# Optimization experiments

Hardware: AMD Instinct MI355X
Metric: run time of the kernel (lower is better)

## Reference

```python
import jax, jax.numpy as jnp
import numpy as np

B, T = 128, 512
V, E, H, A, L = 50000, 256, 512, 64, 2


def setup_inputs() -> dict:
    key = jax.random.key(0)
    ks = jax.random.split(key, 16)
    token_ids = jax.random.randint(ks[0], (B, T), 0, V, dtype=jnp.int32)
    # lengths must be >= 2 so that the source's (len-1)-1 index is valid
    lengths = jnp.clip(jax.random.randint(ks[1], (B,), 0, T, dtype=jnp.int32), 4, T)
    s = 0.05
    inp = {
        "token_ids": token_ids,
        "lengths": lengths,
        "embedding": jax.random.normal(ks[2], (V, E), jnp.float32) * s,
        "Wt": jax.random.normal(ks[3], (A, E), jnp.float32) * s,   # tokens_linear
        "bt": jax.random.normal(ks[4], (A,), jnp.float32) * s,
        "Wq": jax.random.normal(ks[5], (A, H), jnp.float32) * s,   # query_linear
        "bq": jax.random.normal(ks[6], (A,), jnp.float32) * s,
        "v": jax.random.normal(ks[7], (A,), jnp.float32) * s,      # attention_linear weight
        "bv": jax.random.normal(ks[8], (), jnp.float32) * s,       # attention_linear bias
        "gru_Wih0": jax.random.normal(ks[9], (3 * H, A), jnp.float32) * s,
        "gru_Whh0": jax.random.normal(ks[10], (3 * H, H), jnp.float32) * s,
        "gru_bih0": jax.random.normal(ks[11], (3 * H,), jnp.float32) * s,
        "gru_bhh0": jax.random.normal(ks[12], (3 * H,), jnp.float32) * s,
        "gru_Wih1": jax.random.normal(ks[13], (3 * H, H), jnp.float32) * s,
        "gru_Whh1": jax.random.normal(ks[14], (3 * H, H), jnp.float32) * s,
        "gru_bih1": jax.random.normal(ks[15], (3 * H,), jnp.float32) * s,
        "gru_bhh1": jax.random.normal(jax.random.fold_in(key, 99), (3 * H,), jnp.float32) * s,
    }
    return inp


def _gru_cell(x, h, Wih, Whh, bih, bhh):
    gi = x @ Wih.T + bih      # [B, 3H]
    gh = h @ Whh.T + bhh      # [B, 3H]
    i_r, i_z, i_n = jnp.split(gi, 3, axis=-1)
    h_r, h_z, h_n = jnp.split(gh, 3, axis=-1)
    r = jax.nn.sigmoid(i_r + h_r)
    z = jax.nn.sigmoid(i_z + h_z)
    n = jnp.tanh(i_n + r * h_n)
    return (1.0 - z) * n + z * h


def reference(token_ids, lengths, embedding, Wt, bt, Wq, bq, v, bv,
              gru_Wih0, gru_Whh0, gru_bih0, gru_bhh0,
              gru_Wih1, gru_Whh1, gru_bih1, gru_bhh1):
    x = embedding[token_ids]                 # [B, T, E]
    tp = jnp.einsum('bte,ae->bta', x, Wt) + bt   # tokens_linear, [B, T, A]
    pos = jnp.arange(T)

    def step(h, i):
        # query = hidden_state[-1] (zeros at step 0, matching hidden_state=None)
        q = h[-1] @ Wq.T + bq                # [B, A]
        s = jnp.tanh(tp + q[:, None, :]) @ v + bv   # [B, T]
        s = jnp.where(pos[None, :] <= i, s, -jnp.inf)  # growing prefix
        attn = jax.nn.softmax(s, axis=1)
        ctx = jnp.einsum('bt,bta->ba', attn, tp)     # [B, A]
        h0 = _gru_cell(ctx, h[0], gru_Wih0, gru_Whh0, gru_bih0, gru_bhh0)
        h1 = _gru_cell(h0, h[1], gru_Wih1, gru_Whh1, gru_bih1, gru_bhh1)
        return jnp.stack([h0, h1]), h1

    h_init = jnp.zeros((L, B, H), tp.dtype)
    _, outs = jax.lax.scan(step, h_init, jnp.arange(T))   # outs: [T, B, H]
    # source: sequence_lengths = len-1, then index sequence_lengths-1 = len-2
    idx = jnp.clip(lengths - 2, 0, T - 1)
    result = outs[idx, jnp.arange(B)]                     # [B, H]
    return result
```

## Files before the change

kernel.cpp:

```cpp
#include <hip/hip_runtime.h>

#define NB 128
#define NT 512
#define NE 256
#define NH 512
#define NA 64
#define NG 8
#define GB 16

typedef short bf16x8 __attribute__((ext_vector_type(8)));
typedef float f32x4 __attribute__((ext_vector_type(4)));
typedef unsigned short u16x8 __attribute__((ext_vector_type(8)));
typedef unsigned long long u64;

__device__ __forceinline__ unsigned short f2bf(float f){
  unsigned u = __builtin_bit_cast(unsigned, f);
  u = u + 0x7fffu + ((u >> 16) & 1u);
  return (unsigned short)(u >> 16);
}
__device__ __forceinline__ float bf2f(unsigned short h){
  unsigned u = ((unsigned)h) << 16;
  return __builtin_bit_cast(float, u);
}
__device__ __forceinline__ bf16x8 packbf2(f32x4 a, f32x4 b){
  bf16x8 r;
  r[0]=(short)f2bf(a[0]); r[1]=(short)f2bf(a[1]); r[2]=(short)f2bf(a[2]); r[3]=(short)f2bf(a[3]);
  r[4]=(short)f2bf(b[0]); r[5]=(short)f2bf(b[1]); r[6]=(short)f2bf(b[2]); r[7]=(short)f2bf(b[3]);
  return r;
}
__device__ __forceinline__ bf16x8 loadB_f32(const float* p){
  f32x4 a = *(const f32x4*)p;
  f32x4 b = *(const f32x4*)(p + 4);
  return packbf2(a, b);
}
#define MFMA(a,b,c) __builtin_amdgcn_mfma_f32_16x16x32_bf16(a,b,c,0,0,0)

__device__ __forceinline__ float fsig(float x){
  return __builtin_amdgcn_rcpf(1.f + __expf(-x));
}
__device__ __forceinline__ float ftanh(float x){
  float e2 = __expf(2.f * x);
  return 1.f - 2.f * __builtin_amdgcn_rcpf(e2 + 1.f);
}

__device__ __forceinline__ void sleep_bk(int bk){
  if (bk <= 0)      __builtin_amdgcn_s_sleep(1);
  else if (bk == 1) __builtin_amdgcn_s_sleep(2);
  else if (bk == 2) __builtin_amdgcn_s_sleep(4);
  else              __builtin_amdgcn_s_sleep(8);
}

__device__ __forceinline__ u64 aload(const u64* p){
  return __hip_atomic_load(p, __ATOMIC_RELAXED, __HIP_MEMORY_SCOPE_AGENT);
}
__device__ __forceinline__ void fire(u64* p, u64 v){
  (void)__hip_atomic_exchange(p, v, __ATOMIC_RELAXED, __HIP_MEMORY_SCOPE_AGENT);
}
__device__ __forceinline__ u64 packh(unsigned sq, float a, float b){
  return ((u64)sq << 32) | ((u64)f2bf(b) << 16) | (u64)f2bf(a);
}
__device__ __forceinline__ u64 packf(unsigned sq, float a){
  return ((u64)sq << 32) | (u64)__builtin_bit_cast(unsigned, a);
}

__global__ __launch_bounds__(256) void k_tp(
    const int* __restrict__ tok, const float* __restrict__ emb,
    const float* __restrict__ Wt, const float* __restrict__ bt,
    unsigned short* __restrict__ tp)
{
  const int lane = threadIdx.x & 63;
  const int w = threadIdx.x >> 6;
  const int m16 = lane & 15, quad = lane >> 4;

  bf16x8 wfq[8][4];
#pragma unroll
  for (int kc = 0; kc < 8; kc++)
#pragma unroll
    for (int nt = 0; nt < 4; nt++)
      wfq[kc][nt] = loadB_f32(Wt + (nt*16 + m16)*NE + kc*32 + quad*8);

  float btv[4];
#pragma unroll
  for (int nt = 0; nt < 4; nt++) btv[nt] = bt[nt*16 + m16];

  const int gw = blockIdx.x * 4 + w;
#pragma unroll 1
  for (int it = 0; it < 4; it++){
    const int pt = gw * 4 + it;
    const int pos = pt*16 + m16;
    const long row = (long)tok[pos];
    const float* xrow = emb + row * NE;
    f32x4 acc[4] = {{0,0,0,0},{0,0,0,0},{0,0,0,0},{0,0,0,0}};
#pragma unroll
    for (int kc = 0; kc < 8; kc++){
      bf16x8 af = loadB_f32(xrow + kc*32 + quad*8);
#pragma unroll
      for (int nt = 0; nt < 4; nt++)
        acc[nt] = MFMA(af, wfq[kc][nt], acc[nt]);
    }
#pragma unroll
    for (int nt = 0; nt < 4; nt++)
#pragma unroll
      for (int r = 0; r < 4; r++){
        int posr = pt*16 + quad*4 + r;
        tp[(long)posr * NA + nt*16 + m16] = f2bf(acc[nt][r] + btv[nt]);
      }
  }
}

__global__ __launch_bounds__(256) void k_pack(
    const float* __restrict__ Wq, unsigned short* __restrict__ blob)
{
  const int lane = threadIdx.x & 63, wv = threadIdx.x >> 6;
  const int m16 = lane & 15, quad = lane >> 4;
#pragma unroll
  for (int kc = 0; kc < 16; kc++){
    bf16x8 t = loadB_f32(Wq + (long)(wv*16 + m16)*NH + kc*32 + quad*8);
    *(bf16x8*)&blob[((wv*16 + kc)*64 + lane)*8] = t;
  }
}

struct KArgs {
  const int* len;
  const float* bq; const float* v; const float* bv;
  const float* Wih0; const float* Whh0; const float* bih0; const float* bhh0;
  const float* Wih1; const float* Whh1; const float* bih1; const float* bhh1;
  const unsigned short* tp;
  const unsigned short* wqblob;
  u64* hbuf;
  u64* cbuf;
  float* out;
};

__device__ __forceinline__ void stage_load(const u64* __restrict__ buf, unsigned sq,
                                           unsigned short (*hs)[64][8], int tid){
  const int lane = tid & 63, wv = tid >> 6;
  const int b = lane & 15, q8 = lane >> 4;
#pragma unroll
  for (int c = 0; c < 4; c++){
    const int kc = wv*4 + c;
    const u64* u0 = buf + (kc*4 + q8)*64 + b*4;
    u64 x0, x1, x2, x3;
    int bk = 0;
    for (;;){
      x0 = aload(u0);     x1 = aload(u0 + 1);
      x2 = aload(u0 + 2); x3 = aload(u0 + 3);
      if ((unsigned)(x0>>32)==sq && (unsigned)(x1>>32)==sq &&
          (unsigned)(x2>>32)==sq && (unsigned)(x3>>32)==sq) break;
      sleep_bk(bk);
      if (bk < 3) bk++;
    }
    u16x8 d;
    d[0]=(unsigned short)x0; d[1]=(unsigned short)(x0>>16);
    d[2]=(unsigned short)x1; d[3]=(unsigned short)(x1>>16);
    d[4]=(unsigned short)x2; d[5]=(unsigned short)(x2>>16);
    d[6]=(unsigned short)x3; d[7]=(unsigned short)(x3>>16);
    *(u16x8*)&hs[kc][lane][0] = d;
  }
}

__global__ __launch_bounds__(256, 1) void k_main(KArgs A_)
{
  const int tid = threadIdx.x, lane = tid & 63, w = tid >> 6;
  const int g = blockIdx.x & 7, m = blockIdx.x >> 3;
  const int m16 = lane & 15, quad = lane >> 4;

  __shared__ __attribute__((aligned(16))) unsigned short h0s[16][64][8];
  __shared__ __attribute__((aligned(16))) unsigned short h1s[16][64][8];
  __shared__ __attribute__((aligned(16))) float dslab[6][256];
  __shared__ __attribute__((aligned(16))) float qs[16][68];
  __shared__ __attribute__((aligned(16))) float cslab[4][64];
  __shared__ float cden[4];
  __shared__ __attribute__((aligned(16))) unsigned short ctxf[64][16];

  u64* hb = A_.hbuf + (long)g * (4*4096);
  u64* cb = A_.cbuf + (long)g * (2*2*16*72);
  const int b0 = g * GB;

  bf16x8 wf[48], wih0f[2];
  float bhh0v[4], bih0v[4], bhh1v[4], bih1v[4];
  if (w < 3){
    const int r0 = w * NH + m * 16;
#pragma unroll
    for (int kc = 0; kc < 16; kc++){
      wf[kc]    = loadB_f32(A_.Whh0 + (long)(r0 + m16)*NH + kc*32 + quad*8);
      wf[16+kc] = loadB_f32(A_.Whh1 + (long)(r0 + m16)*NH + kc*32 + quad*8);
      wf[32+kc] = loadB_f32(A_.Wih1 + (long)(r0 + m16)*NH + kc*32 + quad*8);
    }
#pragma unroll
    for (int kc = 0; kc < 2; kc++)
      wih0f[kc] = loadB_f32(A_.Wih0 + (r0 + m16)*NA + kc*32 + quad*8);
#pragma unroll
    for (int r = 0; r < 4; r++){
      int d = r0 + quad*4 + r;
      bhh0v[r] = A_.bhh0[d]; bih0v[r] = A_.bih0[d];
      bhh1v[r] = A_.bhh1[d]; bih1v[r] = A_.bih1[d];
    }
  }
  float bqw[4];
#pragma unroll
  for (int r = 0; r < 4; r++) bqw[r] = A_.bq[w*16 + quad*4 + r];

  float vv[16];
#pragma unroll
  for (int jj = 0; jj < 16; jj++) vv[jj] = A_.v[quad*16 + jj];
  const float bvv = A_.bv[0];
  const int ab = m >> 1;
  const int wr = (m & 1)*4 + w;

  int myidx = 0, imax = 0;
#pragma unroll 1
  for (int b = 0; b < GB; b++){
    int L = A_.len[b0 + b];
    int ix = L - 2; ix = ix < 0 ? 0 : (ix > NT-1 ? NT-1 : ix);
    if (b == m16) myidx = ix;
    imax = imax > ix ? imax : ix;
  }

  f32x4 h0p = {0,0,0,0}, h1p = {0,0,0,0};

  {
    u16x8 z = {0,0,0,0,0,0,0,0};
#pragma unroll
    for (int c = 0; c < 4; c++){
      int kc = (tid>>6)*4 + c;
      *(u16x8*)&h0s[kc][lane][0] = z;
      *(u16x8*)&h1s[kc][lane][0] = z;
    }
  }
  __syncthreads();

#pragma unroll 1
  for (int i = 0; i <= imax; i++){
    const int par = i & 1;
    const unsigned sq = (unsigned)(i + 1);

    f32x4 g0 = {0,0,0,0};
    if (w < 3){
#pragma unroll
      for (int kc = 0; kc < 16; kc++){
        bf16x8 h0f = *(const bf16x8*)&h0s[kc][lane][0];
        g0 = MFMA(wf[kc], h0f, g0);
      }
#pragma unroll
      for (int r = 0; r < 4; r++) g0[r] += bhh0v[r];
    }
    if (i > 0){
      stage_load(hb + (long)(2 + ((i-1)&1))*4096, (unsigned)i, h1s, tid);
      __syncthreads();
    }
    {
      f32x4 qa = {0,0,0,0};
#pragma unroll
      for (int kc = 0; kc < 16; kc++){
        bf16x8 b1f = *(const bf16x8*)&h1s[kc][lane][0];
        bf16x8 af = *(const bf16x8*)&A_.wqblob[((w*16 + kc)*64 + lane)*8];
        qa = MFMA(af, b1f, qa);
      }
#pragma unroll
      for (int r = 0; r < 4; r++)
        qs[m16][w*16 + quad*4 + r] = qa[r] + bqw[r];
    }
    __syncthreads();

    {
      float qv[16];
#pragma unroll
      for (int jq = 0; jq < 4; jq++){
        f32x4 t = *(const f32x4*)&qs[ab][quad*16 + jq*4];
        qv[jq*4+0]=t[0]; qv[jq*4+1]=t[1]; qv[jq*4+2]=t[2]; qv[jq*4+3]=t[3];
      }
      float ctxp[16];
#pragma unroll
      for (int jj = 0; jj < 16; jj++) ctxp[jj] = 0.f;
      float denp = 0.f;
      const unsigned short* tpb = A_.tp + (long)(b0 + ab) * NT * NA;
#pragma unroll 1
      for (int c = wr; c*16 <= i; c += 8){
        const int t = c*16 + m16;
        const unsigned short* tpp = tpb + (long)t*NA + quad*16;
        u16x8 ta = *(const u16x8*)tpp;
        u16x8 tb = *(const u16x8*)(tpp + 8);
        float tpf[16];
#pragma unroll
        for (int jj = 0; jj < 8; jj++){ tpf[jj] = bf2f(ta[jj]); tpf[8+jj] = bf2f(tb[jj]); }
        float sp = 0.f;
#pragma unroll
        for (int jj = 0; jj < 16; jj++){
          float x = tpf[jj] + qv[jj];
          sp = fmaf(ftanh(x), vv[jj], sp);
        }
        sp += __shfl_xor(sp, 16);
        sp += __shfl_xor(sp, 32);
        float e = __expf(sp + bvv);
        e = (t <= i) ? e : 0.f;
        denp += e;
#pragma unroll
        for (int jj = 0; jj < 16; jj++) ctxp[jj] = fmaf(e, tpf[jj], ctxp[jj]);
      }
#pragma unroll
      for (int off = 1; off < 64; off <<= 1) denp += __shfl_xor(denp, off);
      denp *= 0.25f;
#pragma unroll
      for (int st = 0; st < 4; st++){
        const int bit = 1 << st;
        const bool up = (lane >> st) & 1;
        const int n2 = (16 >> st) >> 1;
#pragma unroll
        for (int j2 = 0; j2 < 8; j2++){
          if (j2 < n2){
            float keep = up ? ctxp[2*j2+1] : ctxp[2*j2];
            float send = up ? ctxp[2*j2]   : ctxp[2*j2+1];
            float got = __shfl_xor(send, bit);
            ctxp[j2] = keep + got;
          }
        }
      }
      cslab[w][lane] = ctxp[0];
      if (lane == 0) cden[w] = denp;
    }
    __syncthreads();
    if (w == 0){
      float s = cslab[0][lane] + cslab[1][lane] + cslab[2][lane] + cslab[3][lane];
      u64* slot = cb + ((long)(par*2 + (m & 1))*16 + ab)*72;
      fire(slot + lane, packf(sq, s));
      if (lane == 0)
        fire(slot + 64, packf(sq, cden[0]+cden[1]+cden[2]+cden[3]));
    }

    if (w == 3){
      const u64* c0 = cb + ((long)(par*2 + 0)*16 + m16)*72;
      const u64* c1 = cb + ((long)(par*2 + 1)*16 + m16)*72;
      u64 d0, d1;
      {
        int bk = 0;
        for (;;){
          d0 = aload(c0 + 64); d1 = aload(c1 + 64);
          if ((unsigned)(d0>>32)==sq && (unsigned)(d1>>32)==sq) break;
          sleep_bk(bk);
          if (bk < 3) bk++;
        }
      }
      const float rdn = __builtin_amdgcn_rcpf(
          __builtin_bit_cast(float,(unsigned)d0) + __builtin_bit_cast(float,(unsigned)d1));
#pragma unroll
      for (int kc = 0; kc < 2; kc++){
        const int a0 = kc*32 + quad*8;
        u64 t0[8], t1[8];
        int bk = 0;
        for (;;){
          bool ok = true;
#pragma unroll
          for (int j = 0; j < 8; j++){ t0[j] = aload(c0 + a0 + j); ok &= ((unsigned)(t0[j]>>32)==sq); }
#pragma unroll
          for (int j = 0; j < 8; j++){ t1[j] = aload(c1 + a0 + j); ok &= ((unsigned)(t1[j]>>32)==sq); }
          if (ok) break;
          sleep_bk(bk);
          if (bk < 3) bk++;
        }
        u16x8 f;
#pragma unroll
        for (int j = 0; j < 8; j++){
          float s = (__builtin_bit_cast(float,(unsigned)t0[j]) +
                     __builtin_bit_cast(float,(unsigned)t1[j])) * rdn;
          f[j] = f2bf(s);
        }
        *(u16x8*)&ctxf[lane][kc*8] = f;
      }
    }
    __syncthreads();
    if (w < 3){
      f32x4 gi0 = {0,0,0,0};
      bf16x8 cf0 = *(const bf16x8*)&ctxf[lane][0];
      bf16x8 cf1 = *(const bf16x8*)&ctxf[lane][8];
      gi0 = MFMA(wih0f[0], cf0, gi0);
      gi0 = MFMA(wih0f[1], cf1, gi0);
#pragma unroll
      for (int r = 0; r < 4; r++) gi0[r] += bih0v[r];
      *(f32x4*)&dslab[w][lane*4] = g0;
      *(f32x4*)&dslab[3+w][lane*4] = gi0;
    }
    __syncthreads();
    if (w == 3){
      f32x4 ghr = *(f32x4*)&dslab[0][lane*4];
      f32x4 ghz = *(f32x4*)&dslab[1][lane*4];
      f32x4 ghn = *(f32x4*)&dslab[2][lane*4];
      f32x4 gir = *(f32x4*)&dslab[3][lane*4];
      f32x4 giz = *(f32x4*)&dslab[4][lane*4];
      f32x4 gin = *(f32x4*)&dslab[5][lane*4];
      f32x4 hn;
#pragma unroll
      for (int r = 0; r < 4; r++){
        float rr = fsig(gir[r] + ghr[r]);
        float zz = fsig(giz[r] + ghz[r]);
        float nn = ftanh(gin[r] + rr*ghn[r]);
        hn[r] = (1.f - zz)*nn + zz*h0p[r];
      }
      h0p = hn;
      const int dp0 = m*8 + quad*2;
      u64* p0 = hb + (long)par*4096 + (dp0>>2)*64 + m16*4 + (dp0&3);
      fire(p0,     packh(sq, hn[0], hn[1]));
      fire(p0 + 1, packh(sq, hn[2], hn[3]));
    }

    f32x4 gh1 = {0,0,0,0};
    if (w < 3){
#pragma unroll
      for (int kc = 0; kc < 16; kc++){
        bf16x8 b1f = *(const bf16x8*)&h1s[kc][lane][0];
        gh1 = MFMA(wf[16+kc], b1f, gh1);
      }
#pragma unroll
      for (int r = 0; r < 4; r++) gh1[r] += bhh1v[r];
    }
    stage_load(hb + (long)par*4096, sq, h0s, tid);
    __syncthreads();
    if (w < 3){
      f32x4 gi1 = {0,0,0,0};
#pragma unroll
      for (int kc = 0; kc < 16; kc++){
        bf16x8 hf = *(const bf16x8*)&h0s[kc][lane][0];
        gi1 = MFMA(wf[32+kc], hf, gi1);
      }
#pragma unroll
      for (int r = 0; r < 4; r++) gi1[r] += bih1v[r];
      *(f32x4*)&dslab[w][lane*4] = gh1;
      *(f32x4*)&dslab[3+w][lane*4] = gi1;
    }
    __syncthreads();
    if (w == 3){
      f32x4 ghr = *(f32x4*)&dslab[0][lane*4];
      f32x4 ghz = *(f32x4*)&dslab[1][lane*4];
      f32x4 ghn = *(f32x4*)&dslab[2][lane*4];
      f32x4 gir = *(f32x4*)&dslab[3][lane*4];
      f32x4 giz = *(f32x4*)&dslab[4][lane*4];
      f32x4 gin = *(f32x4*)&dslab[5][lane*4];
      f32x4 hn;
#pragma unroll
      for (int r = 0; r < 4; r++){
        float rr = fsig(gir[r] + ghr[r]);
        float zz = fsig(giz[r] + ghz[r]);
        float nn = ftanh(gin[r] + rr*ghn[r]);
        hn[r] = (1.f - zz)*nn + zz*h1p[r];
      }
      h1p = hn;
      const int dp0 = m*8 + quad*2;
      u64* p1 = hb + (long)(2 + par)*4096 + (dp0>>2)*64 + m16*4 + (dp0&3);
      fire(p1,     packh(sq, hn[0], hn[1]));
      fire(p1 + 1, packh(sq, hn[2], hn[3]));
      if (i == myidx)
        *(f32x4*)&A_.out[(long)(b0 + m16)*NH + m*16 + quad*4] = hn;
    }
  }
}

extern "C" void kernel_launch(void* const* d_in, const int* in_sizes, int n_in,
                              void* d_out, int out_size, void* d_ws, size_t ws_size,
                              hipStream_t stream)
{
  (void)in_sizes; (void)n_in; (void)out_size; (void)ws_size;
  char* ws = (char*)d_ws;
  unsigned short* tp     = (unsigned short*)ws;
  unsigned short* wqblob = (unsigned short*)(ws + 8388608);
  u64* hbuf = (u64*)(ws + 8388608 + 65536);
  u64* cbuf = hbuf + 8 * (4*4096);

  (void)hipMemsetAsync(hbuf, 0xFF, (size_t)(8*4*4096 + 8*2*2*16*72) * sizeof(u64), stream);

  k_tp<<<dim3(256), dim3(256), 0, stream>>>(
      (const int*)d_in[0], (const float*)d_in[2], (const float*)d_in[3],
      (const float*)d_in[4], tp);
  k_pack<<<dim3(1), dim3(256), 0, stream>>>((const float*)d_in[5], wqblob);

  KArgs ka;
  ka.len  = (const int*)d_in[1];
  ka.bq   = (const float*)d_in[6];
  ka.v    = (const float*)d_in[7];  ka.bv   = (const float*)d_in[8];
  ka.Wih0 = (const float*)d_in[9];  ka.Whh0 = (const float*)d_in[10];
  ka.bih0 = (const float*)d_in[11]; ka.bhh0 = (const float*)d_in[12];
  ka.Wih1 = (const float*)d_in[13]; ka.Whh1 = (const float*)d_in[14];
  ka.bih1 = (const float*)d_in[15]; ka.bhh1 = (const float*)d_in[16];
  ka.tp = tp; ka.wqblob = wqblob;
  ka.hbuf = hbuf; ka.cbuf = cbuf;
  ka.out = (float*)d_out;

  k_main<<<dim3(256), dim3(256), 0, stream>>>(ka);
}
```

Measured before the change: 6.863 ms.

## Halve block count, double waves per block to cut cross-block context exchange

```diff
diff --git a/kernel.cpp b/kernel.cpp
--- a/kernel.cpp
+++ b/kernel.cpp
@@ -134,32 +134,37 @@
 
 __device__ __forceinline__ void stage_load(const u64* __restrict__ buf, unsigned sq,
                                            unsigned short (*hs)[64][8], int tid){
-  const int lane = tid & 63, wv = tid >> 6;
+  const int lane = tid & 63, w8 = tid >> 6;
   const int b = lane & 15, q8 = lane >> 4;
-#pragma unroll
-  for (int c = 0; c < 4; c++){
-    const int kc = wv*4 + c;
-    const u64* u0 = buf + (kc*4 + q8)*64 + b*4;
-    u64 x0, x1, x2, x3;
-    int bk = 0;
-    for (;;){
-      x0 = aload(u0);     x1 = aload(u0 + 1);
-      x2 = aload(u0 + 2); x3 = aload(u0 + 3);
-      if ((unsigned)(x0>>32)==sq && (unsigned)(x1>>32)==sq &&
-          (unsigned)(x2>>32)==sq && (unsigned)(x3>>32)==sq) break;
-      sleep_bk(bk);
-      if (bk < 3) bk++;
-    }
-    u16x8 d;
-    d[0]=(unsigned short)x0; d[1]=(unsigned short)(x0>>16);
-    d[2]=(unsigned short)x1; d[3]=(unsigned short)(x1>>16);
-    d[4]=(unsigned short)x2; d[5]=(unsigned short)(x2>>16);
-    d[6]=(unsigned short)x3; d[7]=(unsigned short)(x3>>16);
-    *(u16x8*)&hs[kc][lane][0] = d;
-  }
-}
-
-__global__ __launch_bounds__(256, 1) void k_main(KArgs A_)
+  const u64* uA = buf + ((w8*2+0)*4 + q8)*64 + b*4;
+  const u64* uB = buf + ((w8*2+1)*4 + q8)*64 + b*4;
+  u64 x[8];
+  int bk = 0;
+  for (;;){
+    bool ok = true;
+#pragma unroll
+    for (int j = 0; j < 4; j++) x[j]   = aload(uA + j);
+#pragma unroll
+    for (int j = 0; j < 4; j++) x[4+j] = aload(uB + j);
+#pragma unroll
+    for (int j = 0; j < 8; j++) ok &= ((unsigned)(x[j]>>32) == sq);
+    if (ok) break;
+    sleep_bk(bk);
+    if (bk < 3) bk++;
+  }
+  u16x8 dA, dB;
+#pragma unroll
+  for (int j = 0; j < 4; j++){
+    dA[2*j]   = (unsigned short)x[j];
+    dA[2*j+1] = (unsigned short)(x[j] >> 16);
+    dB[2*j]   = (unsigned short)x[4+j];
+    dB[2*j+1] = (unsigned short)(x[4+j] >> 16);
+  }
+  *(u16x8*)&hs[w8*2+0][lane][0] = dA;
+  *(u16x8*)&hs[w8*2+1][lane][0] = dB;
+}
+
+__global__ __launch_bounds__(512, 1) void k_main(KArgs A_)
 {
   const int tid = threadIdx.x, lane = tid & 63, w = tid >> 6;
   const int g = blockIdx.x & 7, m = blockIdx.x >> 3;
@@ -167,20 +172,20 @@
 
   __shared__ __attribute__((aligned(16))) unsigned short h0s[16][64][8];
   __shared__ __attribute__((aligned(16))) unsigned short h1s[16][64][8];
-  __shared__ __attribute__((aligned(16))) float dslab[6][256];
+  __shared__ __attribute__((aligned(16))) float dslab[6][512];
   __shared__ __attribute__((aligned(16))) float qs[16][68];
-  __shared__ __attribute__((aligned(16))) float cslab[4][64];
-  __shared__ float cden[4];
+  __shared__ __attribute__((aligned(16))) float cslab[8][64];
+  __shared__ float cden[8];
   __shared__ __attribute__((aligned(16))) unsigned short ctxf[64][16];
 
   u64* hb = A_.hbuf + (long)g * (4*4096);
-  u64* cb = A_.cbuf + (long)g * (2*2*16*72);
+  u64* cb = A_.cbuf + (long)g * (2*16*72);
   const int b0 = g * GB;
 
   bf16x8 wf[48], wih0f[2];
   float bhh0v[4], bih0v[4], bhh1v[4], bih1v[4];
-  if (w < 3){
-    const int r0 = w * NH + m * 16;
+  if (w < 6){
+    const int r0 = (w % 3) * NH + m * 32 + (w / 3) * 16;
 #pragma unroll
     for (int kc = 0; kc < 16; kc++){
       wf[kc]    = loadB_f32(A_.Whh0 + (long)(r0 + m16)*NH + kc*32 + quad*8);
@@ -199,14 +204,12 @@
   }
   float bqw[4];
 #pragma unroll
-  for (int r = 0; r < 4; r++) bqw[r] = A_.bq[w*16 + quad*4 + r];
+  for (int r = 0; r < 4; r++) bqw[r] = A_.bq[(w & 3)*16 + quad*4 + r];
 
   float vv[16];
 #pragma unroll
   for (int jj = 0; jj < 16; jj++) vv[jj] = A_.v[quad*16 + jj];
   const float bvv = A_.bv[0];
-  const int ab = m >> 1;
-  const int wr = (m & 1)*4 + w;
 
   int myidx = 0, imax = 0;
 #pragma unroll 1
@@ -222,8 +225,8 @@
   {
     u16x8 z = {0,0,0,0,0,0,0,0};
 #pragma unroll
-    for (int c = 0; c < 4; c++){
-      int kc = (tid>>6)*4 + c;
+    for (int c = 0; c < 2; c++){
+      int kc = w*2 + c;
       *(u16x8*)&h0s[kc][lane][0] = z;
       *(u16x8*)&h1s[kc][lane][0] = z;
     }
@@ -236,7 +239,7 @@
     const unsigned sq = (unsigned)(i + 1);
 
     f32x4 g0 = {0,0,0,0};
-    if (w < 3){
+    if (w < 6){
 #pragma unroll
       for (int kc = 0; kc < 16; kc++){
         bf16x8 h0f = *(const bf16x8*)&h0s[kc][lane][0];
@@ -245,11 +248,10 @@
 #pragma unroll
       for (int r = 0; r < 4; r++) g0[r] += bhh0v[r];
     }
-    if (i > 0){
+    if (i > 0)
       stage_load(hb + (long)(2 + ((i-1)&1))*4096, (unsigned)i, h1s, tid);
-      __syncthreads();
-    }
-    {
+    __syncthreads();
+    if (w < 4){
       f32x4 qa = {0,0,0,0};
 #pragma unroll
       for (int kc = 0; kc < 16; kc++){
@@ -267,16 +269,16 @@
       float qv[16];
 #pragma unroll
       for (int jq = 0; jq < 4; jq++){
-        f32x4 t = *(const f32x4*)&qs[ab][quad*16 + jq*4];
+        f32x4 t = *(const f32x4*)&qs[m][quad*16 + jq*4];
         qv[jq*4+0]=t[0]; qv[jq*4+1]=t[1]; qv[jq*4+2]=t[2]; qv[jq*4+3]=t[3];
       }
       float ctxp[16];
 #pragma unroll
       for (int jj = 0; jj < 16; jj++) ctxp[jj] = 0.f;
       float denp = 0.f;
-      const unsigned short* tpb = A_.tp + (long)(b0 + ab) * NT * NA;
+      const unsigned short* tpb = A_.tp + (long)(b0 + m) * NT * NA;
 #pragma unroll 1
-      for (int c = wr; c*16 <= i; c += 8){
+      for (int c = w; c*16 <= i; c += 8){
         const int t = c*16 + m16;
         const unsigned short* tpp = tpb + (long)t*NA + quad*16;
         u16x8 ta = *(const u16x8*)tpp;
@@ -321,55 +323,42 @@
     }
     __syncthreads();
     if (w == 0){
-      float s = cslab[0][lane] + cslab[1][lane] + cslab[2][lane] + cslab[3][lane];
-      u64* slot = cb + ((long)(par*2 + (m & 1))*16 + ab)*72;
+      float s = cslab[0][lane] + cslab[1][lane] + cslab[2][lane] + cslab[3][lane]
+              + cslab[4][lane] + cslab[5][lane] + cslab[6][lane] + cslab[7][lane];
+      u64* slot = cb + ((long)par*16 + m)*72;
       fire(slot + lane, packf(sq, s));
-      if (lane == 0)
-        fire(slot + 64, packf(sq, cden[0]+cden[1]+cden[2]+cden[3]));
-    }
-
-    if (w == 3){
-      const u64* c0 = cb + ((long)(par*2 + 0)*16 + m16)*72;
-      const u64* c1 = cb + ((long)(par*2 + 1)*16 + m16)*72;
-      u64 d0, d1;
-      {
-        int bk = 0;
-        for (;;){
-          d0 = aload(c0 + 64); d1 = aload(c1 + 64);
-          if ((unsigned)(d0>>32)==sq && (unsigned)(d1>>32)==sq) break;
-          sleep_bk(bk);
-          if (bk < 3) bk++;
-        }
-      }
-      const float rdn = __builtin_amdgcn_rcpf(
-          __builtin_bit_cast(float,(unsigned)d0) + __builtin_bit_cast(float,(unsigned)d1));
-#pragma unroll
-      for (int kc = 0; kc < 2; kc++){
-        const int a0 = kc*32 + quad*8;
-        u64 t0[8], t1[8];
-        int bk = 0;
-        for (;;){
-          bool ok = true;
-#pragma unroll
-          for (int j = 0; j < 8; j++){ t0[j] = aload(c0 + a0 + j); ok &= ((unsigned)(t0[j]>>32)==sq); }
-#pragma unroll
-          for (int j = 0; j < 8; j++){ t1[j] = aload(c1 + a0 + j); ok &= ((unsigned)(t1[j]>>32)==sq); }
-          if (ok) break;
-          sleep_bk(bk);
-          if (bk < 3) bk++;
-        }
-        u16x8 f;
-#pragma unroll
-        for (int j = 0; j < 8; j++){
-          float s = (__builtin_bit_cast(float,(unsigned)t0[j]) +
-                     __builtin_bit_cast(float,(unsigned)t1[j])) * rdn;
-          f[j] = f2bf(s);
-        }
-        *(u16x8*)&ctxf[lane][kc*8] = f;
-      }
-    }
-    __syncthreads();
-    if (w < 3){
+      if (lane == 0){
+        float dsum = cden[0]+cden[1]+cden[2]+cden[3]+cden[4]+cden[5]+cden[6]+cden[7];
+        fire(slot + 64, packf(sq, dsum));
+      }
+    }
+
+    if (w >= 6){
+      const int kc = w - 6;
+      const u64* c0 = cb + ((long)par*16 + m16)*72;
+      u64 dn, t[8];
+      int bk = 0;
+      for (;;){
+        bool ok = true;
+        dn = aload(c0 + 64);
+#pragma unroll
+        for (int j = 0; j < 8; j++) t[j] = aload(c0 + kc*32 + quad*8 + j);
+        ok = ((unsigned)(dn>>32) == sq);
+#pragma unroll
+        for (int j = 0; j < 8; j++) ok &= ((unsigned)(t[j]>>32) == sq);
+        if (ok) break;
+        sleep_bk(bk);
+        if (bk < 3) bk++;
+      }
+      const float rdn = __builtin_amdgcn_rcpf(__builtin_bit_cast(float, (unsigned)dn));
+      u16x8 f;
+#pragma unroll
+      for (int j = 0; j < 8; j++)
+        f[j] = f2bf(__builtin_bit_cast(float, (unsigned)t[j]) * rdn);
+      *(u16x8*)&ctxf[lane][kc*8] = f;
+    }
+    __syncthreads();
+    if (w < 6){
       f32x4 gi0 = {0,0,0,0};
       bf16x8 cf0 = *(const bf16x8*)&ctxf[lane][0];
       bf16x8 cf1 = *(const bf16x8*)&ctxf[lane][8];
@@ -377,17 +366,19 @@
       gi0 = MFMA(wih0f[1], cf1, gi0);
 #pragma unroll
       for (int r = 0; r < 4; r++) gi0[r] += bih0v[r];
-      *(f32x4*)&dslab[w][lane*4] = g0;
-      *(f32x4*)&dslab[3+w][lane*4] = gi0;
-    }
-    __syncthreads();
-    if (w == 3){
-      f32x4 ghr = *(f32x4*)&dslab[0][lane*4];
-      f32x4 ghz = *(f32x4*)&dslab[1][lane*4];
-      f32x4 ghn = *(f32x4*)&dslab[2][lane*4];
-      f32x4 gir = *(f32x4*)&dslab[3][lane*4];
-      f32x4 giz = *(f32x4*)&dslab[4][lane*4];
-      f32x4 gin = *(f32x4*)&dslab[5][lane*4];
+      const int off = (w/3)*256 + lane*4;
+      *(f32x4*)&dslab[w%3][off] = g0;
+      *(f32x4*)&dslab[3 + w%3][off] = gi0;
+    }
+    __syncthreads();
+    if (w >= 6){
+      const int off = (w-6)*256 + lane*4;
+      f32x4 ghr = *(f32x4*)&dslab[0][off];
+      f32x4 ghz = *(f32x4*)&dslab[1][off];
+      f32x4 ghn = *(f32x4*)&dslab[2][off];
+      f32x4 gir = *(f32x4*)&dslab[3][off];
+      f32x4 giz = *(f32x4*)&dslab[4][off];
+      f32x4 gin = *(f32x4*)&dslab[5][off];
       f32x4 hn;
 #pragma unroll
       for (int r = 0; r < 4; r++){
@@ -397,14 +388,14 @@
         hn[r] = (1.f - zz)*nn + zz*h0p[r];
       }
       h0p = hn;
-      const int dp0 = m*8 + quad*2;
+      const int dp0 = m*16 + (w-6)*8 + quad*2;
       u64* p0 = hb + (long)par*4096 + (dp0>>2)*64 + m16*4 + (dp0&3);
       fire(p0,     packh(sq, hn[0], hn[1]));
       fire(p0 + 1, packh(sq, hn[2], hn[3]));
     }
 
     f32x4 gh1 = {0,0,0,0};
-    if (w < 3){
+    if (w < 6){
 #pragma unroll
       for (int kc = 0; kc < 16; kc++){
         bf16x8 b1f = *(const bf16x8*)&h1s[kc][lane][0];
@@ -415,7 +406,7 @@
     }
     stage_load(hb + (long)par*4096, sq, h0s, tid);
     __syncthreads();
-    if (w < 3){
+    if (w < 6){
       f32x4 gi1 = {0,0,0,0};
 #pragma unroll
       for (int kc = 0; kc < 16; kc++){
@@ -424,17 +415,19 @@
       }
 #pragma unroll
       for (int r = 0; r < 4; r++) gi1[r] += bih1v[r];
-      *(f32x4*)&dslab[w][lane*4] = gh1;
-      *(f32x4*)&dslab[3+w][lane*4] = gi1;
-    }
-    __syncthreads();
-    if (w == 3){
-      f32x4 ghr = *(f32x4*)&dslab[0][lane*4];
-      f32x4 ghz = *(f32x4*)&dslab[1][lane*4];
-      f32x4 ghn = *(f32x4*)&dslab[2][lane*4];
-      f32x4 gir = *(f32x4*)&dslab[3][lane*4];
-      f32x4 giz = *(f32x4*)&dslab[4][lane*4];
-      f32x4 gin = *(f32x4*)&dslab[5][lane*4];
+      const int off = (w/3)*256 + lane*4;
+      *(f32x4*)&dslab[w%3][off] = gh1;
+      *(f32x4*)&dslab[3 + w%3][off] = gi1;
+    }
+    __syncthreads();
+    if (w >= 6){
+      const int off = (w-6)*256 + lane*4;
+      f32x4 ghr = *(f32x4*)&dslab[0][off];
+      f32x4 ghz = *(f32x4*)&dslab[1][off];
+      f32x4 ghn = *(f32x4*)&dslab[2][off];
+      f32x4 gir = *(f32x4*)&dslab[3][off];
+      f32x4 giz = *(f32x4*)&dslab[4][off];
+      f32x4 gin = *(f32x4*)&dslab[5][off];
       f32x4 hn;
 #pragma unroll
       for (int r = 0; r < 4; r++){
@@ -444,12 +437,12 @@
         hn[r] = (1.f - zz)*nn + zz*h1p[r];
       }
       h1p = hn;
-      const int dp0 = m*8 + quad*2;
+      const int dp0 = m*16 + (w-6)*8 + quad*2;
       u64* p1 = hb + (long)(2 + par)*4096 + (dp0>>2)*64 + m16*4 + (dp0&3);
       fire(p1,     packh(sq, hn[0], hn[1]));
       fire(p1 + 1, packh(sq, hn[2], hn[3]));
       if (i == myidx)
-        *(f32x4*)&A_.out[(long)(b0 + m16)*NH + m*16 + quad*4] = hn;
+        *(f32x4*)&A_.out[(long)(b0 + m16)*NH + m*32 + (w-6)*16 + quad*4] = hn;
     }
   }
 }
@@ -465,7 +458,7 @@
   u64* hbuf = (u64*)(ws + 8388608 + 65536);
   u64* cbuf = hbuf + 8 * (4*4096);
 
-  (void)hipMemsetAsync(hbuf, 0xFF, (size_t)(8*4*4096 + 8*2*2*16*72) * sizeof(u64), stream);
+  (void)hipMemsetAsync(hbuf, 0xFF, (size_t)(8*4*4096 + 8*2*16*72) * sizeof(u64), stream);
 
   k_tp<<<dim3(256), dim3(256), 0, stream>>>(
       (const int*)d_in[0], (const float*)d_in[2], (const float*)d_in[3],
@@ -484,5 +477,5 @@
   ka.hbuf = hbuf; ka.cbuf = cbuf;
   ka.out = (float*)d_out;
 
-  k_main<<<dim3(256), dim3(256), 0, stream>>>(ka);
-}
+  k_main<<<dim3(128), dim3(512), 0, stream>>>(ka);
+}
```

New measurement: 8.889 ms. 29.5% more time.
